# Kernel optimization log

Measured on AMD Instinct MI355X. Metric: run time of the kernel, lower is better.

The kernel has to match this reference:

```python
import jax, jax.numpy as jnp
import numpy as np

BN_EPS = 1e-5


def setup_inputs() -> dict:
    key = jax.random.key(0)
    ks = jax.random.split(key, 12)
    N, F, H, E, ED, G, EMB = 59392, 116, 256, 950272, 5, 8, 16
    return {
        "x": jax.random.normal(ks[0], (N, F), dtype=jnp.float32),
        "edge_index": jax.random.randint(ks[1], (2, E), 0, N, dtype=jnp.int64),
        "edge_attr": jax.random.normal(ks[2], (E, ED), dtype=jnp.float32),
        "group_ids": jax.random.randint(ks[3], (N,), 0, G, dtype=jnp.int64),
        "group_emb": jax.random.normal(ks[4], (G, EMB), dtype=jnp.float32),
        "W_in": jax.random.normal(ks[5], (F + EMB, H), dtype=jnp.float32) * 0.05,
        "b_in": jnp.zeros((H,), dtype=jnp.float32),
        "gamma": jnp.ones((H,), dtype=jnp.float32),
        "beta": jnp.zeros((H,), dtype=jnp.float32),
        "We": jax.random.normal(ks[6], (ED, H), dtype=jnp.float32) * 0.05,
        "be": jnp.zeros((H,), dtype=jnp.float32),
        "W1": jax.random.normal(ks[7], (H, H), dtype=jnp.float32) * 0.05,
        "b1": jnp.zeros((H,), dtype=jnp.float32),
        "W2": jax.random.normal(ks[8], (H, H), dtype=jnp.float32) * 0.05,
        "b2": jnp.zeros((H,), dtype=jnp.float32),
    }


def reference(x, edge_index, edge_attr, group_ids, group_emb, W_in, b_in,
              gamma, beta, We, be, W1, b1, W2, b2):
    N = x.shape[0]
    # group-embedding concat (dropout is identity in eval mode)
    h = jnp.concatenate([x, group_emb[group_ids]], axis=-1)      # [N, F+EMB]
    # dynamically-created Linear + ReLU
    h = jax.nn.relu(h @ W_in + b_in)                              # [N, H]
    # BatchNorm over nodes (training stats, biased var)
    mu = jnp.mean(h, axis=0)
    var = jnp.mean(jnp.square(h - mu), axis=0)
    h = (h - mu) * jax.lax.rsqrt(var + BN_EPS) * gamma + beta
    # GINEConv: msg = ReLU(x_j + lin(edge_attr)); sum-aggregate at target
    src, dst = edge_index[0], edge_index[1]
    msg = jax.nn.relu(h[src] + edge_attr @ We + be)               # [E, H]
    agg = jax.ops.segment_sum(msg, dst, num_segments=N)          # [N, H]
    z = h + agg                                                   # (1+eps)*h, eps=0
    out = jax.nn.relu(z @ W1 + b1) @ W2 + b2                      # 2-layer MLP
    out = jax.nn.relu(out)
    return (out, edge_attr)
```

## Files before the change

kernel.cpp:

```cpp
#include <hip/hip_runtime.h>
#include <hip/hip_bf16.h>
#include <cstdint>
#include <cstddef>

#define H 256
#define EMB 16
#define ED 5
#define BN_EPS 1e-5f
#define CAP 48

typedef __attribute__((ext_vector_type(8))) short short8;
typedef __attribute__((ext_vector_type(4))) float f32x4;
typedef _Float16 h2 __attribute__((ext_vector_type(2)));

__device__ __forceinline__ unsigned short f2bf(float f) {
  unsigned int u = __float_as_uint(f);
  unsigned int r = (u + 0x7fffu + ((u >> 16) & 1u)) >> 16;
  return (unsigned short)r;
}
__device__ __forceinline__ unsigned int pk2bf(float a, float b) {
  return (unsigned int)f2bf(a) | ((unsigned int)f2bf(b) << 16);
}
__device__ __forceinline__ unsigned short f2h(float f) {
  union { _Float16 h; unsigned short u; } c;
  c.h = (_Float16)f;
  return c.u;
}
__device__ __forceinline__ h2 u2h2(unsigned int u) {
  union { unsigned int u; h2 h; } c;
  c.u = u;
  return c.h;
}
__device__ __forceinline__ unsigned int h22u(h2 h) {
  union { h2 h; unsigned int u; } c;
  c.h = h;
  return c.u;
}
__device__ __forceinline__ h2 mkh2(float a, float b) {
  h2 r;
  r.x = (_Float16)a;
  r.y = (_Float16)b;
  return r;
}

__global__ __launch_bounds__(256) void prep_kernel(
    const float* __restrict__ Win, const float* __restrict__ W1,
    const float* __restrict__ W2, const float* __restrict__ gemb,
    const float* __restrict__ b_in, unsigned short* __restrict__ Wtx,
    unsigned short* __restrict__ Wt1, unsigned short* __restrict__ Wt2,
    float* __restrict__ T, float* __restrict__ stats, int* __restrict__ cnt,
    int N, int F, int G) {
  int idx = blockIdx.x * 256 + threadIdx.x;
  if (idx < 1024) stats[idx] = 0.f;
  if (idx < N) cnt[idx] = 0;
  if (idx < 256 * 128) {
    int n = idx >> 7, k = idx & 127;
    Wtx[idx] = f2bf((k < F) ? Win[(size_t)k * H + n] : 0.f);
  } else if (idx < 256 * 128 + 65536) {
    int i2 = idx - 256 * 128;
    int n = i2 >> 8, k = i2 & 255;
    Wt1[i2] = f2bf(W1[(size_t)k * H + n]);
  } else if (idx < 256 * 128 + 131072) {
    int i2 = idx - 256 * 128 - 65536;
    int n = i2 >> 8, k = i2 & 255;
    Wt2[i2] = f2bf(W2[(size_t)k * H + n]);
  } else if (idx < 256 * 128 + 131072 + G * 256) {
    int i2 = idx - 256 * 128 - 131072;
    int g = i2 >> 8, c = i2 & 255;
    float s = b_in[c];
    #pragma unroll
    for (int k = 0; k < EMB; ++k)
      s = fmaf(gemb[g * EMB + k], Win[(size_t)(F + k) * H + c], s);
    T[i2] = s;
  }
}

__global__ __launch_bounds__(256) void scatter_gemm_kernel(
    const int* __restrict__ ei, const float* __restrict__ ea,
    int* __restrict__ cnt, uint4* __restrict__ rec,
    float* __restrict__ ea_out, int E,
    const float* __restrict__ x, const int* __restrict__ gid,
    const unsigned short* __restrict__ Wtx, const float* __restrict__ T,
    unsigned short* __restrict__ h0, float* __restrict__ stats,
    int F, int GB) {
  __shared__ __align__(16) unsigned short As[128][40];
  __shared__ __align__(16) unsigned short Bs[128][40];
  __shared__ float cs[128], css[128];
  const int bid = blockIdx.x;
  const int tid = threadIdx.x;
  const bool isG = ((bid % 5) == 4) && (bid / 5 < GB);
  if (!isG) {
    const int nG = min((bid + 1) / 5, GB);
    const int sb = bid - nG;
    int e = sb * 256 + tid;
    if (e >= E) return;
    int s = ei[e];
    int d = ei[E + e];
    const float* eap = ea + (size_t)e * ED;
    const float e0 = eap[0], e1 = eap[1], e2 = eap[2], e3 = eap[3],
                e4 = eap[4];
    int p = atomicAdd(&cnt[d], 1);
    if (p >= CAP) p = CAP - 1;
    uint4 r;
    r.x = ((unsigned)s) << 9;
    r.y = h22u(mkh2(e0, e1));
    r.z = h22u(mkh2(e2, e3));
    r.w = h22u(mkh2(e4, 0.f));
    rec[(size_t)d * CAP + p] = r;
    float* op = ea_out + (size_t)e * ED;
    op[0] = e0; op[1] = e1; op[2] = e2; op[3] = e3; op[4] = e4;
    return;
  }
  const int gidx = bid / 5;
  const int m0 = (gidx >> 1) * 128;
  const int n0 = (gidx & 1) * 128;
  const int lane = tid & 63;
  const int wave = tid >> 6;
  const int wm = (wave & 1) * 64;
  const int wn = (wave >> 1) * 64;
  const int l16 = lane & 15;
  const int quad = lane >> 4;
  if (tid < 128) {
    cs[tid] = 0.f;
    css[tid] = 0.f;
  }
  f32x4 acc[4][4] = {};
  const int srow = tid >> 1;
  const int half = tid & 1;
  for (int k0 = 0; k0 < 128; k0 += 32) {
    __syncthreads();
    {
      const float* xp = x + (size_t)(m0 + srow) * F;
      float4 xv[4];
      #pragma unroll
      for (int f = 0; f < 4; ++f) {
        int c = k0 + half * 16 + f * 4;
        xv[f] = (c < F) ? *(const float4*)(xp + c)
                        : make_float4(0.f, 0.f, 0.f, 0.f);
      }
      uint4 p0, p1;
      p0.x = pk2bf(xv[0].x, xv[0].y); p0.y = pk2bf(xv[0].z, xv[0].w);
      p0.z = pk2bf(xv[1].x, xv[1].y); p0.w = pk2bf(xv[1].z, xv[1].w);
      p1.x = pk2bf(xv[2].x, xv[2].y); p1.y = pk2bf(xv[2].z, xv[2].w);
      p1.z = pk2bf(xv[3].x, xv[3].y); p1.w = pk2bf(xv[3].z, xv[3].w);
      *(uint4*)(&As[srow][half * 16]) = p0;
      *(uint4*)(&As[srow][half * 16 + 8]) = p1;
    }
    {
      const unsigned short* wp = Wtx + (size_t)(n0 + srow) * 128 + k0 + half * 16;
      *(uint4*)(&Bs[srow][half * 16]) = *(const uint4*)wp;
      *(uint4*)(&Bs[srow][half * 16 + 8]) = *(const uint4*)(wp + 8);
    }
    __syncthreads();
    short8 af[4], bf[4];
    #pragma unroll
    for (int i = 0; i < 4; ++i)
      af[i] = *(const short8*)(&As[wm + i * 16 + l16][quad * 8]);
    #pragma unroll
    for (int j = 0; j < 4; ++j)
      bf[j] = *(const short8*)(&Bs[wn + j * 16 + l16][quad * 8]);
    #pragma unroll
    for (int i = 0; i < 4; ++i)
      #pragma unroll
      for (int j = 0; j < 4; ++j)
        acc[i][j] = __builtin_amdgcn_mfma_f32_16x16x32_bf16(af[i], bf[j],
                                                            acc[i][j], 0, 0, 0);
  }
  int gi[4][4];
  #pragma unroll
  for (int i = 0; i < 4; ++i)
    #pragma unroll
    for (int r = 0; r < 4; ++r)
      gi[i][r] = gid[m0 + wm + i * 16 + quad * 4 + r];
  float ls[4] = {}, lss[4] = {};
  #pragma unroll
  for (int j = 0; j < 4; ++j) {
    const int col = n0 + wn + j * 16 + l16;
    #pragma unroll
    for (int i = 0; i < 4; ++i) {
      #pragma unroll
      for (int r = 0; r < 4; ++r) {
        const int row = m0 + wm + i * 16 + quad * 4 + r;
        float v = fmaxf(acc[i][j][r] + T[gi[i][r] * H + col], 0.f);
        h0[(size_t)row * H + col] = f2h(v);
        ls[j] += v;
        lss[j] = fmaf(v, v, lss[j]);
      }
    }
  }
  #pragma unroll
  for (int j = 0; j < 4; ++j) {
    const int lc = wn + j * 16 + l16;
    atomicAdd(&cs[lc], ls[j]);
    atomicAdd(&css[lc], lss[j]);
  }
  __syncthreads();
  if (tid < 128) {
    atomicAdd(&stats[n0 + tid], cs[tid]);
    atomicAdd(&stats[H + n0 + tid], css[tid]);
  }
}

__global__ __launch_bounds__(256) void mlp_kernel(
    const unsigned short* __restrict__ z, const unsigned short* __restrict__ Wt1,
    const unsigned short* __restrict__ Wt2, const float* __restrict__ b1,
    const float* __restrict__ b2, float* __restrict__ out) {
  const int m0 = blockIdx.x * 64;
  const int tid = threadIdx.x;
  const int lane = tid & 63;
  const int wave = tid >> 6;
  const int wn = wave * 64;
  const int l16 = lane & 15;
  const int quad = lane >> 4;
  __shared__ __align__(16) unsigned short As[64][40];
  __shared__ __align__(16) unsigned short Bs[256][40];
  __shared__ __align__(16) unsigned short hidS[64][264];
  f32x4 acc[4][4] = {};
  const int ar = tid >> 2, ac = tid & 3;
  for (int k0 = 0; k0 < 256; k0 += 32) {
    __syncthreads();
    *(float4*)(&As[ar][ac * 8]) =
        *(const float4*)(z + (size_t)(m0 + ar) * H + k0 + ac * 8);
    #pragma unroll
    for (int t = 0; t < 4; ++t) {
      int r = ar + t * 64;
      *(float4*)(&Bs[r][ac * 8]) =
          *(const float4*)(Wt1 + (size_t)r * H + k0 + ac * 8);
    }
    __syncthreads();
    short8 af[4], bf[4];
    #pragma unroll
    for (int i = 0; i < 4; ++i)
      af[i] = *(const short8*)(&As[i * 16 + l16][quad * 8]);
    #pragma unroll
    for (int j = 0; j < 4; ++j)
      bf[j] = *(const short8*)(&Bs[wn + j * 16 + l16][quad * 8]);
    #pragma unroll
    for (int i = 0; i < 4; ++i)
      #pragma unroll
      for (int j = 0; j < 4; ++j)
        acc[i][j] = __builtin_amdgcn_mfma_f32_16x16x32_bf16(af[i], bf[j],
                                                            acc[i][j], 0, 0, 0);
  }
  #pragma unroll
  for (int j = 0; j < 4; ++j) {
    const int col = wn + j * 16 + l16;
    const float bj = b1[col];
    #pragma unroll
    for (int i = 0; i < 4; ++i)
      #pragma unroll
      for (int r = 0; r < 4; ++r) {
        const int row = i * 16 + quad * 4 + r;
        hidS[row][col] = f2bf(fmaxf(acc[i][j][r] + bj, 0.f));
      }
  }
  #pragma unroll
  for (int i = 0; i < 4; ++i)
    #pragma unroll
    for (int j = 0; j < 4; ++j)
      acc[i][j] = (f32x4){0.f, 0.f, 0.f, 0.f};
  for (int k0 = 0; k0 < 256; k0 += 32) {
    __syncthreads();
    #pragma unroll
    for (int t = 0; t < 4; ++t) {
      int r = ar + t * 64;
      *(float4*)(&Bs[r][ac * 8]) =
          *(const float4*)(Wt2 + (size_t)r * H + k0 + ac * 8);
    }
    __syncthreads();
    short8 af[4], bf[4];
    #pragma unroll
    for (int i = 0; i < 4; ++i)
      af[i] = *(const short8*)(&hidS[i * 16 + l16][k0 + quad * 8]);
    #pragma unroll
    for (int j = 0; j < 4; ++j)
      bf[j] = *(const short8*)(&Bs[wn + j * 16 + l16][quad * 8]);
    #pragma unroll
    for (int i = 0; i < 4; ++i)
      #pragma unroll
      for (int j = 0; j < 4; ++j)
        acc[i][j] = __builtin_amdgcn_mfma_f32_16x16x32_bf16(af[i], bf[j],
                                                            acc[i][j], 0, 0, 0);
  }
  #pragma unroll
  for (int j = 0; j < 4; ++j) {
    const int col = wn + j * 16 + l16;
    const float bj = b2[col];
    #pragma unroll
    for (int i = 0; i < 4; ++i)
      #pragma unroll
      for (int r = 0; r < 4; ++r) {
        const int row = m0 + i * 16 + quad * 4 + r;
        out[(size_t)row * H + col] = fmaxf(acc[i][j][r] + bj, 0.f);
      }
  }
}

__device__ __forceinline__ void edge_accum(
    const uint4 rr, const uint2 hv, const h2 aA, const h2 aB,
    const h2 bA, const h2 bB, const h2 wA[5], const h2 wB[5],
    float& ax, float& ay, float& az, float& aw) {
  h2 m01 = aA * u2h2(hv.x) + bA;
  h2 m23 = aB * u2h2(hv.y) + bB;
  const h2 e01 = u2h2(rr.y), e23 = u2h2(rr.z), e44 = u2h2(rr.w);
  h2 t;
  t.x = e01.x; t.y = e01.x;  m01 += t * wA[0]; m23 += t * wB[0];
  t.x = e01.y; t.y = e01.y;  m01 += t * wA[1]; m23 += t * wB[1];
  t.x = e23.x; t.y = e23.x;  m01 += t * wA[2]; m23 += t * wB[2];
  t.x = e23.y; t.y = e23.y;  m01 += t * wA[3]; m23 += t * wB[3];
  t.x = e44.x; t.y = e44.x;  m01 += t * wA[4]; m23 += t * wB[4];
  const h2 z2 = {(_Float16)0.f, (_Float16)0.f};
  m01 = __builtin_elementwise_max(m01, z2);
  m23 = __builtin_elementwise_max(m23, z2);
  ax += (float)m01.x;
  ay += (float)m01.y;
  az += (float)m23.x;
  aw += (float)m23.y;
}

__global__ __launch_bounds__(256) void aggregate_kernel(
    const unsigned short* __restrict__ h0, const uint4* __restrict__ rec,
    const float* __restrict__ We, const float* __restrict__ be,
    const float* __restrict__ gamma, const float* __restrict__ beta,
    const float* __restrict__ stats, const int* __restrict__ cntv,
    unsigned short* __restrict__ z, int N, float inv_n) {
  const int lane = threadIdx.x & 63;
  int n = blockIdx.x * 4 + (threadIdx.x >> 6);
  if (n >= N) return;
  n = __builtin_amdgcn_readfirstlane(n);
  const int c = lane * 4;
  const int c2 = c << 1;
  const float4 be4 = *(const float4*)(be + c);
  h2 aA, aB, bA, bB;
  {
    const float4 s1v = *(const float4*)(stats + c);
    const float4 s2v = *(const float4*)(stats + H + c);
    const float4 g4 = *(const float4*)(gamma + c);
    const float4 bt4 = *(const float4*)(beta + c);
    float a[4], b[4];
    float m0 = s1v.x * inv_n, m1 = s1v.y * inv_n,
          m2 = s1v.z * inv_n, m3 = s1v.w * inv_n;
    a[0] = g4.x / sqrtf(s2v.x * inv_n - m0 * m0 + BN_EPS);
    a[1] = g4.y / sqrtf(s2v.y * inv_n - m1 * m1 + BN_EPS);
    a[2] = g4.z / sqrtf(s2v.z * inv_n - m2 * m2 + BN_EPS);
    a[3] = g4.w / sqrtf(s2v.w * inv_n - m3 * m3 + BN_EPS);
    b[0] = bt4.x - m0 * a[0] + be4.x;
    b[1] = bt4.y - m1 * a[1] + be4.y;
    b[2] = bt4.z - m2 * a[2] + be4.z;
    b[3] = bt4.w - m3 * a[3] + be4.w;
    aA = mkh2(a[0], a[1]); aB = mkh2(a[2], a[3]);
    bA = mkh2(b[0], b[1]); bB = mkh2(b[2], b[3]);
  }
  h2 wA[5], wB[5];
  #pragma unroll
  for (int k = 0; k < 5; ++k) {
    wA[k] = mkh2(We[k * H + c], We[k * H + c + 1]);
    wB[k] = mkh2(We[k * H + c + 2], We[k * H + c + 3]);
  }
  float ax = 0.f, ay = 0.f, az = 0.f, aw = 0.f;
  int cnt = __builtin_amdgcn_readfirstlane(cntv[n]);
  cnt = (cnt < CAP) ? cnt : CAP;
  const uint4* rp = rec + (size_t)n * CAP;
  const char* hb = (const char*)h0;
  int i = 0;
  for (; i + 8 <= cnt; i += 8) {
    uint4 rr[8];
    uint2 hh[8];
    #pragma unroll
    for (int u = 0; u < 8; ++u) rr[u] = rp[i + u];
    #pragma unroll
    for (int u = 0; u < 8; ++u)
      hh[u] = *(const uint2*)(hb + rr[u].x + c2);
    #pragma unroll
    for (int u = 0; u < 8; ++u)
      edge_accum(rr[u], hh[u], aA, aB, bA, bB, wA, wB, ax, ay, az, aw);
  }
  for (; i + 4 <= cnt; i += 4) {
    uint4 rr[4];
    uint2 hh[4];
    #pragma unroll
    for (int u = 0; u < 4; ++u) rr[u] = rp[i + u];
    #pragma unroll
    for (int u = 0; u < 4; ++u)
      hh[u] = *(const uint2*)(hb + rr[u].x + c2);
    #pragma unroll
    for (int u = 0; u < 4; ++u)
      edge_accum(rr[u], hh[u], aA, aB, bA, bB, wA, wB, ax, ay, az, aw);
  }
  for (; i < cnt; ++i) {
    const uint4 r0 = rp[i];
    const uint2 h0v = *(const uint2*)(hb + r0.x + c2);
    edge_accum(r0, h0v, aA, aB, bA, bB, wA, wB, ax, ay, az, aw);
  }
  const uint2 hs = *(const uint2*)(h0 + (size_t)n * H + c);
  const h2 s01 = aA * u2h2(hs.x) + bA;
  const h2 s23 = aB * u2h2(hs.y) + bB;
  float zx = (float)s01.x - be4.x + ax;
  float zy = (float)s01.y - be4.y + ay;
  float zz = (float)s23.x - be4.z + az;
  float zw = (float)s23.y - be4.w + aw;
  uint2 o;
  o.x = pk2bf(zx, zy);
  o.y = pk2bf(zz, zw);
  *(uint2*)(z + (size_t)n * H + c) = o;
}

extern "C" void kernel_launch(void* const* d_in, const int* in_sizes, int n_in,
                              void* d_out, int out_size, void* d_ws, size_t ws_size,
                              hipStream_t stream) {
  const float* x     = (const float*)d_in[0];
  const int*   ei    = (const int*)d_in[1];
  const float* ea    = (const float*)d_in[2];
  const int*   gid   = (const int*)d_in[3];
  const float* gemb  = (const float*)d_in[4];
  const float* W_in  = (const float*)d_in[5];
  const float* b_in  = (const float*)d_in[6];
  const float* gamma = (const float*)d_in[7];
  const float* beta  = (const float*)d_in[8];
  const float* We    = (const float*)d_in[9];
  const float* be    = (const float*)d_in[10];
  const float* W1    = (const float*)d_in[11];
  const float* b1    = (const float*)d_in[12];
  const float* W2    = (const float*)d_in[13];
  const float* b2    = (const float*)d_in[14];
  float* out = (float*)d_out;

  const int N = in_sizes[3];
  const int E = in_sizes[1] / 2;
  const int F = in_sizes[0] / N;
  const int G = in_sizes[4] / EMB;

  char* p = (char*)d_ws;
  auto take = [&](size_t bytes) {
    char* r = p;
    p += (bytes + 255) & ~(size_t)255;
    return r;
  };
  float* stats          = (float*)take(1024 * sizeof(float));
  int* cnt              = (int*)take((size_t)N * 4);
  uint4* rec            = (uint4*)take((size_t)N * CAP * 16);
  unsigned short* Wtx   = (unsigned short*)take((size_t)256 * 128 * 2);
  unsigned short* Wt1   = (unsigned short*)take((size_t)H * H * 2);
  unsigned short* Wt2   = (unsigned short*)take((size_t)H * H * 2);
  float* T              = (float*)take((size_t)G * H * 4);
  unsigned short* h0    = (unsigned short*)take((size_t)N * H * 2);
  unsigned short* z     = (unsigned short*)take((size_t)N * H * 2);

  {
    int total = 256 * 128 + 131072 + G * 256;
    int nb = (total + 255) / 256;
    if (nb < (N + 255) / 256) nb = (N + 255) / 256;
    prep_kernel<<<nb, 256, 0, stream>>>(W_in, W1, W2, gemb, b_in, Wtx, Wt1,
                                        Wt2, T, stats, cnt, N, F, G);
  }

  {
    const int SB = (E + 255) / 256;
    const int GB = (N / 128) * (H / 128);
    scatter_gemm_kernel<<<SB + GB, 256, 0, stream>>>(
        ei, ea, cnt, rec, out + (size_t)N * H, E,
        x, gid, Wtx, T, h0, stats, F, GB);
  }

  aggregate_kernel<<<(N + 3) / 4, 256, 0, stream>>>(
      h0, rec, We, be, gamma, beta, stats, cnt, z, N, 1.0f / (float)N);

  mlp_kernel<<<N / 64, 256, 0, stream>>>(z, Wt1, Wt2, b1, b2, out);
}
```

Before: 321.3 us.

## Process two edges per scatter thread, rebalance interleave, load MLP A-fragments directly

Each scatter thread now handles two edges, issuing both loads and both atomics before the record writes. This halves the scatter block count, so the interleave ratio of GEMM to scatter blocks changes from 1:4 to 1:2. In the MLP kernel, the first GEMM reads its A fragments straight from global memory instead of staging them in shared memory, and the LDS row padding is reduced. A sync is added before hidS is written, since the B-tile buffer could still be in use. The reduced padding (36 and 260 shorts) may raise LDS bank conflicts.

```diff
diff --git a/kernel.cpp b/kernel.cpp
--- a/kernel.cpp
+++ b/kernel.cpp
@@ -88,30 +88,57 @@
   __shared__ float cs[128], css[128];
   const int bid = blockIdx.x;
   const int tid = threadIdx.x;
-  const bool isG = ((bid % 5) == 4) && (bid / 5 < GB);
+  const bool isG = ((bid % 3) == 2) && (bid / 3 < GB);
   if (!isG) {
-    const int nG = min((bid + 1) / 5, GB);
+    const int nG = min((bid + 1) / 3, GB);
     const int sb = bid - nG;
-    int e = sb * 256 + tid;
-    if (e >= E) return;
-    int s = ei[e];
-    int d = ei[E + e];
-    const float* eap = ea + (size_t)e * ED;
-    const float e0 = eap[0], e1 = eap[1], e2 = eap[2], e3 = eap[3],
-                e4 = eap[4];
-    int p = atomicAdd(&cnt[d], 1);
-    if (p >= CAP) p = CAP - 1;
-    uint4 r;
-    r.x = ((unsigned)s) << 9;
-    r.y = h22u(mkh2(e0, e1));
-    r.z = h22u(mkh2(e2, e3));
-    r.w = h22u(mkh2(e4, 0.f));
-    rec[(size_t)d * CAP + p] = r;
-    float* op = ea_out + (size_t)e * ED;
-    op[0] = e0; op[1] = e1; op[2] = e2; op[3] = e3; op[4] = e4;
+    const int e0 = sb * 512 + tid;
+    const int e1 = e0 + 256;
+    int s0v = 0, d0v = 0, s1v = 0, d1v = 0;
+    float a0[ED], a1[ED];
+    const bool v0 = (e0 < E), v1 = (e1 < E);
+    if (v0) {
+      s0v = ei[e0]; d0v = ei[E + e0];
+      const float* p0 = ea + (size_t)e0 * ED;
+      #pragma unroll
+      for (int k = 0; k < ED; ++k) a0[k] = p0[k];
+    }
+    if (v1) {
+      s1v = ei[e1]; d1v = ei[E + e1];
+      const float* p1 = ea + (size_t)e1 * ED;
+      #pragma unroll
+      for (int k = 0; k < ED; ++k) a1[k] = p1[k];
+    }
+    int q0 = 0, q1 = 0;
+    if (v0) q0 = atomicAdd(&cnt[d0v], 1);
+    if (v1) q1 = atomicAdd(&cnt[d1v], 1);
+    if (v0) {
+      if (q0 >= CAP) q0 = CAP - 1;
+      uint4 r;
+      r.x = ((unsigned)s0v) << 9;
+      r.y = h22u(mkh2(a0[0], a0[1]));
+      r.z = h22u(mkh2(a0[2], a0[3]));
+      r.w = h22u(mkh2(a0[4], 0.f));
+      rec[(size_t)d0v * CAP + q0] = r;
+      float* op = ea_out + (size_t)e0 * ED;
+      #pragma unroll
+      for (int k = 0; k < ED; ++k) op[k] = a0[k];
+    }
+    if (v1) {
+      if (q1 >= CAP) q1 = CAP - 1;
+      uint4 r;
+      r.x = ((unsigned)s1v) << 9;
+      r.y = h22u(mkh2(a1[0], a1[1]));
+      r.z = h22u(mkh2(a1[2], a1[3]));
+      r.w = h22u(mkh2(a1[4], 0.f));
+      rec[(size_t)d1v * CAP + q1] = r;
+      float* op = ea_out + (size_t)e1 * ED;
+      #pragma unroll
+      for (int k = 0; k < ED; ++k) op[k] = a1[k];
+    }
     return;
   }
-  const int gidx = bid / 5;
+  const int gidx = bid / 3;
   const int m0 = (gidx >> 1) * 128;
   const int n0 = (gidx & 1) * 128;
   const int lane = tid & 63;
@@ -212,15 +239,12 @@
   const int wn = wave * 64;
   const int l16 = lane & 15;
   const int quad = lane >> 4;
-  __shared__ __align__(16) unsigned short As[64][40];
-  __shared__ __align__(16) unsigned short Bs[256][40];
-  __shared__ __align__(16) unsigned short hidS[64][264];
+  __shared__ __align__(16) unsigned short Bs[256][36];
+  __shared__ __align__(16) unsigned short hidS[64][260];
   f32x4 acc[4][4] = {};
   const int ar = tid >> 2, ac = tid & 3;
   for (int k0 = 0; k0 < 256; k0 += 32) {
     __syncthreads();
-    *(float4*)(&As[ar][ac * 8]) =
-        *(const float4*)(z + (size_t)(m0 + ar) * H + k0 + ac * 8);
     #pragma unroll
     for (int t = 0; t < 4; ++t) {
       int r = ar + t * 64;
@@ -231,7 +255,8 @@
     short8 af[4], bf[4];
     #pragma unroll
     for (int i = 0; i < 4; ++i)
-      af[i] = *(const short8*)(&As[i * 16 + l16][quad * 8]);
+      af[i] = *(const short8*)(z + (size_t)(m0 + i * 16 + l16) * H + k0 +
+                               quad * 8);
     #pragma unroll
     for (int j = 0; j < 4; ++j)
       bf[j] = *(const short8*)(&Bs[wn + j * 16 + l16][quad * 8]);
@@ -242,6 +267,7 @@
         acc[i][j] = __builtin_amdgcn_mfma_f32_16x16x32_bf16(af[i], bf[j],
                                                             acc[i][j], 0, 0, 0);
   }
+  __syncthreads();
   #pragma unroll
   for (int j = 0; j < 4; ++j) {
     const int col = wn + j * 16 + l16;
@@ -455,7 +481,7 @@
   }
 
   {
-    const int SB = (E + 255) / 256;
+    const int SB = (E + 511) / 512;
     const int GB = (N / 128) * (H / 128);
     scatter_gemm_kernel<<<SB + GB, 256, 0, stream>>>(
         ei, ea, cnt, rec, out + (size_t)N * H, E,
```

After: 349.4 us. +8.7%, slower.
